# Kernel tuning notes

Hardware: AMD Instinct MI355X
Metric: run time of the kernel (lower is better)

## Reference

```python
import jax, jax.numpy as jnp
import numpy as np

B, R, T, D = 16, 1024, 512, 1024
H = 1024  # hidden_dim

def setup_inputs() -> dict:
    key = jax.random.key(0)
    ks = jax.random.split(key, 8)
    s_in = 1.0 / np.sqrt(D)
    s_comb = 1.0 / np.sqrt(3 * D)
    return {
        "region_feats": jax.random.normal(ks[0], (B, R, D), jnp.float32),
        "query_embs": jax.random.normal(ks[1], (B, T, D), jnp.float32),
        "Wr": jax.random.normal(ks[2], (D, H), jnp.float32) * s_in,
        "br": jnp.zeros((H,), jnp.float32),
        "Wq": jax.random.normal(ks[3], (D, H), jnp.float32) * s_in,
        "bq": jnp.zeros((H,), jnp.float32),
        "Ws": jax.random.normal(ks[4], (3 * D, 1), jnp.float32) * s_comb,
        "bs": jnp.zeros((1,), jnp.float32),
    }

def reference(region_feats, query_embs, Wr, br, Wq, bq, Ws, bs):
    # Dense projections
    R_proj = region_feats @ Wr + br            # [B,R,H]
    Q_proj = query_embs @ Wq + bq              # [B,T,H]
    # Unscaled cross-attention scores
    scores = jnp.einsum('brd,btd->brt', R_proj, Q_proj)  # [B,R,T]
    attn = jax.nn.softmax(scores, axis=-1)
    # Attend over RAW query embeddings (as in source)
    attended = jnp.einsum('brt,btd->brd', attn, query_embs)  # [B,R,D]
    combined = jnp.concatenate(
        [region_feats, attended, region_feats * attended], axis=-1)  # [B,R,3D]
    out = combined @ Ws + bs                    # [B,R,1]
    return jnp.squeeze(out, axis=-1)            # [B,R]
```

## Files before the change

### kernel.cpp

```cpp
#include <hip/hip_runtime.h>


#define BD 16
#define RD 1024
#define TD 512
#define DD 1024
#define BR (BD * RD)

typedef _Float16 half8 __attribute__((ext_vector_type(8)));
typedef _Float16 half4 __attribute__((ext_vector_type(4)));
typedef float floatx4 __attribute__((ext_vector_type(4)));

__device__ __forceinline__ float wave_sum(float v) {
#pragma unroll
  for (int off = 32; off > 0; off >>= 1) v += __shfl_down(v, off);
  return v;
}

__device__ __forceinline__ half8 cvt8(float4 a, float4 b) {
  half8 h = {(_Float16)a.x, (_Float16)a.y, (_Float16)a.z, (_Float16)a.w,
             (_Float16)b.x, (_Float16)b.y, (_Float16)b.z, (_Float16)b.w};
  return h;
}

__device__ __forceinline__ void gl16(const _Float16* g, _Float16* l) {
  __builtin_amdgcn_global_load_lds(
      (const __attribute__((address_space(1))) void*)g,
      (__attribute__((address_space(3))) void*)l, 16, 0, 0);
}

__global__ __launch_bounds__(256) void prep_all(
    const float* __restrict__ Wr, const float* __restrict__ Wq,
    const float* __restrict__ Ws, const float* __restrict__ br,
    const float* __restrict__ region, const float* __restrict__ query,
    _Float16* __restrict__ M2, _Float16* __restrict__ Ws16,
    float* __restrict__ wqbr, _Float16* __restrict__ wqbr16,
    _Float16* __restrict__ r16, float* __restrict__ rdvec,
    _Float16* __restrict__ q16, float* __restrict__ h1) {
  __shared__ __align__(16) _Float16 lds[2 * 2 * 2048];
  __shared__ float sm[4];
  const int blk = blockIdx.x, tid = threadIdx.x;

  if (blk < 256) {
    const int m0 = (blk >> 4) * 64, n0 = (blk & 15) * 64;
    const int lane = tid & 63, w = tid >> 6;
    const int wr = w >> 1, wc = w & 1;
    const int srow = tid >> 2, slot = tid & 3;
    const int scol = (slot ^ ((srow >> 1) & 3)) * 8;
    const long offA = (long)(m0 + srow) * DD + scol;
    const long offB = (long)(n0 + srow) * DD + scol;
    const int wofs = srow * 32 + slot * 8;
    const int NK = DD / 32;
    float4 a0, a1, b0, b1;
    a0 = *(const float4*)(Wr + offA); a1 = *(const float4*)(Wr + offA + 4);
    b0 = *(const float4*)(Wq + offB); b1 = *(const float4*)(Wq + offB + 4);
    *(int4*)&lds[wofs] = *(int4*)&(const half8&)cvt8(a0, a1);
    {
      half8 hb = cvt8(b0, b1);
      *(half8*)&lds[2048 + wofs] = hb;
    }
    a0 = *(const float4*)(Wr + offA + 32); a1 = *(const float4*)(Wr + offA + 36);
    b0 = *(const float4*)(Wq + offB + 32); b1 = *(const float4*)(Wq + offB + 36);
    __syncthreads();
    floatx4 acc[2][2] = {};
    const int fr = lane & 15, g = lane >> 4;
    const int fs = (g ^ ((fr >> 1) & 3)) * 8;
    for (int kt = 0; kt < NK; ++kt) {
      const int cur = (kt & 1) * 4096, nxt = ((kt + 1) & 1) * 4096;
      if (kt + 1 < NK) {
        half8 ha = cvt8(a0, a1), hb = cvt8(b0, b1);
        *(half8*)&lds[nxt + wofs] = ha;
        *(half8*)&lds[nxt + 2048 + wofs] = hb;
      }
      if (kt + 2 < NK) {
        const long go = (long)(kt + 2) * 32;
        a0 = *(const float4*)(Wr + offA + go); a1 = *(const float4*)(Wr + offA + go + 4);
        b0 = *(const float4*)(Wq + offB + go); b1 = *(const float4*)(Wq + offB + go + 4);
      }
      half8 af[2], bf[2];
#pragma unroll
      for (int i = 0; i < 2; ++i)
        af[i] = *(const half8*)&lds[cur + (32 * wr + 16 * i + fr) * 32 + fs];
#pragma unroll
      for (int j = 0; j < 2; ++j)
        bf[j] = *(const half8*)&lds[cur + 2048 + (32 * wc + 16 * j + fr) * 32 + fs];
#pragma unroll
      for (int i = 0; i < 2; ++i)
#pragma unroll
        for (int j = 0; j < 2; ++j)
          acc[i][j] = __builtin_amdgcn_mfma_f32_16x16x32_f16(af[i], bf[j], acc[i][j], 0, 0, 0);
      __syncthreads();
    }
    const int cr = g * 4, cc = fr;
#pragma unroll
    for (int i = 0; i < 2; ++i)
#pragma unroll
      for (int r = 0; r < 4; ++r)
#pragma unroll
        for (int j = 0; j < 2; ++j)
          M2[(long)(m0 + 32 * wr + 16 * i + cr + r) * DD + n0 + 32 * wc + 16 * j + cc] =
              (_Float16)acc[i][j][r];
  } else if (blk < 258) {
    const long i = (long)(blk - 256) * 1024 + tid * 4;
    const float4 v = *(const float4*)&Ws[DD + i];
    half4 h = {(_Float16)v.x, (_Float16)v.y, (_Float16)v.z, (_Float16)v.w};
    *(half4*)&Ws16[i] = h;
  } else if (blk < 514) {
    const int row = (blk - 258) * 4 + (tid >> 6);
    const int lane = tid & 63;
    const float* x = Wq + (long)row * DD;
    float s = 0.f;
    for (int k = lane; k < DD; k += 64) s += x[k] * br[k];
    s = wave_sum(s);
    if (lane == 0) {
      wqbr[row] = s;
      wqbr16[row] = (_Float16)s;
    }
  } else if (blk < 514 + BR) {
    const long row = blk - 514;
    const int lane = tid & 63, wid = tid >> 6;
    const long i = row * DD + tid * 4;
    const float4 v = *(const float4*)&region[i];
    half4 h = {(_Float16)v.x, (_Float16)v.y, (_Float16)v.z, (_Float16)v.w};
    *(half4*)&r16[i] = h;
    const float4 w0 = *(const float4*)&Ws[tid * 4];
    float rd = v.x * w0.x + v.y * w0.y + v.z * w0.z + v.w * w0.w;
    rd = wave_sum(rd);
    if (lane == 0) sm[wid] = rd;
    __syncthreads();
    if (tid == 0) rdvec[row] = sm[0] + sm[1] + sm[2] + sm[3];
  } else {
    const long row = blk - (514 + BR);
    const int lane = tid & 63, wid = tid >> 6;
    const long i = row * DD + tid * 4;
    const float4 v = *(const float4*)&query[i];
    half4 h = {(_Float16)v.x, (_Float16)v.y, (_Float16)v.z, (_Float16)v.w};
    *(half4*)&q16[i] = h;
    const float4 w1 = *(const float4*)&Ws[DD + tid * 4];
    float hq = v.x * w1.x + v.y * w1.y + v.z * w1.z + v.w * w1.w;
    hq = wave_sum(hq);
    if (lane == 0) sm[wid] = hq;
    __syncthreads();
    if (tid == 0) h1[row] = sm[0] + sm[1] + sm[2] + sm[3];
  }
}

__global__ __launch_bounds__(512, 4) void qp_gemm(
    const _Float16* __restrict__ A, const _Float16* __restrict__ B,
    _Float16* __restrict__ C, const _Float16* __restrict__ wq16,
    float* __restrict__ cvec) {
  __shared__ __align__(16) _Float16 lds[2 * 2 * 4096];
  const int lin = blockIdx.x;
  const int s = lin & 7, u = lin >> 3;
  const int mt = s * 8 + (u >> 3), nt = u & 7;
  const int m0 = mt * 128, n0 = nt * 128;
  const int tid = threadIdx.x, lane = tid & 63, w = tid >> 6;
  const int wr = w >> 1, wc = w & 1;

  const int lrow = lane >> 2, slot = lane & 3;
  const int scol = (slot ^ ((lrow >> 1) & 3)) * 8;
  const int srow = 16 * w + lrow;
  const _Float16* gA = A + (long)(m0 + srow) * DD + scol;
  const _Float16* gB = B + (long)(n0 + srow) * DD + scol;
  const int wbase = 512 * w;

  gl16(gA, &lds[wbase]);
  gl16(gB, &lds[4096 + wbase]);
  __syncthreads();

  floatx4 acc[2][4] = {};
  float cvp[2] = {0.f, 0.f};
  const int fr = lane & 15, g = lane >> 4;
  const int fs = (g ^ ((fr >> 1) & 3)) * 8;
  const int NK = DD / 32;

  for (int kt = 0; kt < NK; ++kt) {
    const int cur = (kt & 1) * 8192, nxt = cur ^ 8192;
    if (kt + 1 < NK) {
      const long go = (long)(kt + 1) * 32;
      gl16(gA + go, &lds[nxt + wbase]);
      gl16(gB + go, &lds[nxt + 4096 + wbase]);
    }
    half8 af[2], bf[4];
#pragma unroll
    for (int i = 0; i < 2; ++i)
      af[i] = *(const half8*)&lds[cur + (32 * wr + 16 * i + fr) * 32 + fs];
#pragma unroll
    for (int j = 0; j < 4; ++j)
      bf[j] = *(const half8*)&lds[cur + 4096 + (64 * wc + 16 * j + fr) * 32 + fs];
    if (wc == 0) {
      const half8 wb = *(const half8*)&wq16[kt * 32 + g * 8];
#pragma unroll
      for (int i = 0; i < 2; ++i)
#pragma unroll
        for (int e = 0; e < 8; ++e)
          cvp[i] += (float)af[i][e] * (float)wb[e];
    }
#pragma unroll
    for (int i = 0; i < 2; ++i)
#pragma unroll
      for (int j = 0; j < 4; ++j)
        acc[i][j] = __builtin_amdgcn_mfma_f32_16x16x32_f16(af[i], bf[j], acc[i][j], 0, 0, 0);
    __syncthreads();
  }

  if (wc == 0 && nt == 0) {
#pragma unroll
    for (int i = 0; i < 2; ++i) {
      float c = cvp[i];
      c += __shfl_xor(c, 16);
      c += __shfl_xor(c, 32);
      if (lane < 16) cvec[m0 + 32 * wr + 16 * i + lane] = c;
    }
  }

  const int cr = g * 4, cc = fr;
#pragma unroll
  for (int i = 0; i < 2; ++i)
#pragma unroll
    for (int r = 0; r < 4; ++r)
#pragma unroll
      for (int j = 0; j < 4; ++j)
        C[(long)(m0 + 32 * wr + 16 * i + cr + r) * DD + n0 + 64 * wc + 16 * j + cc] =
            (_Float16)acc[i][j][r];
}

__global__ __launch_bounds__(512, 4) void gemm_fused(
    const _Float16* __restrict__ A, const _Float16* __restrict__ B0,
    const _Float16* __restrict__ B1,
    float* __restrict__ Ms, float* __restrict__ Ls, float* __restrict__ Hs,
    const float* __restrict__ cvec, const float* __restrict__ h1,
    const _Float16* __restrict__ wsh, long sA, long sB) {
  __shared__ __align__(16) _Float16 lds[2 * 3 * 4096];
  __shared__ __align__(16) _Float16 wlds[1024];

  const int lin = blockIdx.x;
  const int s = lin & 7, u = lin >> 3;
  const int b = 2 * s + (u >> 5);
  const int t = u & 31;
  const int mt = t >> 2, nt = t & 3;
  const int m0 = mt * 128, n0 = nt * 128;
  A += (long)b * sA;
  B0 += (long)b * sB;
  B1 += (long)b * sB;

  const int tid = threadIdx.x, lane = tid & 63, w = tid >> 6;
  const int wr = w >> 2, wc = w & 3;

  const int lrow = lane >> 2, slot = lane & 3;
  const int scol = (slot ^ ((lrow >> 1) & 3)) * 8;
  const int srow = 16 * w + lrow;
  const _Float16* gA = A + (long)(m0 + srow) * DD + scol;
  const _Float16* gP = B0 + (long)(n0 + srow) * DD + scol;
  const _Float16* gQ = B1 + (long)(n0 + srow) * DD + scol;
  const int wbase = 512 * w;

  if (tid < 128) *(int4*)&wlds[tid * 8] = *(const int4*)&wsh[1024 + tid * 8];

  gl16(gA, &lds[wbase]);
  gl16(gP, &lds[4096 + wbase]);
  gl16(gQ, &lds[8192 + wbase]);
  __syncthreads();

  floatx4 accS[4][2] = {};
  floatx4 accH[4][2] = {};
  const int fr = lane & 15, g = lane >> 4;
  const int fs = (g ^ ((fr >> 1) & 3)) * 8;
  const int NK = DD / 32;

  for (int kt = 0; kt < NK; ++kt) {
    const int cur = (kt & 1) * 12288;
    const int nxt = cur ^ 12288;
    if (kt + 1 < NK) {
      const long go = (long)(kt + 1) * 32;
      gl16(gA + go, &lds[nxt + wbase]);
      gl16(gP + go, &lds[nxt + 4096 + wbase]);
      gl16(gQ + go, &lds[nxt + 8192 + wbase]);
    }
    half8 af[4], bp[2], bq[2];
#pragma unroll
    for (int i = 0; i < 4; ++i)
      af[i] = *(const half8*)&lds[cur + (64 * wr + 16 * i + fr) * 32 + fs];
#pragma unroll
    for (int j = 0; j < 2; ++j)
      bp[j] = *(const half8*)&lds[cur + 4096 + (32 * wc + 16 * j + fr) * 32 + fs];
#pragma unroll
    for (int j = 0; j < 2; ++j)
      bq[j] = *(const half8*)&lds[cur + 8192 + (32 * wc + 16 * j + fr) * 32 + fs];
    const half8 w2f = *(const half8*)&wlds[kt * 32 + g * 8];
#pragma unroll
    for (int j = 0; j < 2; ++j) bq[j] *= w2f;
#pragma unroll
    for (int i = 0; i < 4; ++i)
#pragma unroll
      for (int j = 0; j < 2; ++j)
        accS[i][j] = __builtin_amdgcn_mfma_f32_16x16x32_f16(af[i], bp[j], accS[i][j], 0, 0, 0);
#pragma unroll
    for (int i = 0; i < 4; ++i)
#pragma unroll
      for (int j = 0; j < 2; ++j)
        accH[i][j] = __builtin_amdgcn_mfma_f32_16x16x32_f16(af[i], bq[j], accH[i][j], 0, 0, 0);
    __syncthreads();
  }

  const int cr = g * 4, cc = fr;
  float cv[2], hv[2];
#pragma unroll
  for (int j = 0; j < 2; ++j) {
    const long col = (long)b * TD + n0 + 32 * wc + 16 * j + cc;
    cv[j] = cvec[col];
    hv[j] = h1[col];
  }
  const int chunk = nt * 4 + wc;
  const long rowBase = (long)b * RD + m0 + 64 * wr + cr;
#pragma unroll
  for (int i = 0; i < 4; ++i) {
#pragma unroll
    for (int r = 0; r < 4; ++r) {
      float mx = fmaxf(accS[i][0][r] + cv[0], accS[i][1][r] + cv[1]);
      mx = fmaxf(mx, __shfl_xor(mx, 1));
      mx = fmaxf(mx, __shfl_xor(mx, 2));
      mx = fmaxf(mx, __shfl_xor(mx, 4));
      mx = fmaxf(mx, __shfl_xor(mx, 8));
      float l = 0.f, hs = 0.f;
#pragma unroll
      for (int j = 0; j < 2; ++j) {
        const float e = __expf(accS[i][j][r] + cv[j] - mx);
        l += e;
        hs += e * (accH[i][j][r] + hv[j]);
      }
      l += __shfl_xor(l, 1); hs += __shfl_xor(hs, 1);
      l += __shfl_xor(l, 2); hs += __shfl_xor(hs, 2);
      l += __shfl_xor(l, 4); hs += __shfl_xor(hs, 4);
      l += __shfl_xor(l, 8); hs += __shfl_xor(hs, 8);
      if (cc == 0) {
        const long idx = (long)chunk * BR + rowBase + 16 * i + r;
        Ms[idx] = mx;
        Ls[idx] = l;
        Hs[idx] = hs;
      }
    }
  }
}

__global__ __launch_bounds__(256) void combine(
    const float* __restrict__ Ms, const float* __restrict__ Ls,
    const float* __restrict__ Hs, const float* __restrict__ rdvec,
    const float* __restrict__ bs, float* __restrict__ out) {
  const int row = blockIdx.x * 256 + threadIdx.x;
  float mv[16];
  float gm = -1e30f;
#pragma unroll
  for (int c = 0; c < 16; ++c) {
    mv[c] = Ms[(long)c * BR + row];
    gm = fmaxf(gm, mv[c]);
  }
  float L = 0.f, HS = 0.f;
#pragma unroll
  for (int c = 0; c < 16; ++c) {
    const float sc = __expf(mv[c] - gm);
    L += Ls[(long)c * BR + row] * sc;
    HS += Hs[(long)c * BR + row] * sc;
  }
  out[row] = HS / L + rdvec[row] + bs[0];
}

extern "C" void kernel_launch(void* const* d_in, const int* in_sizes, int n_in,
                              void* d_out, int out_size, void* d_ws, size_t ws_size,
                              hipStream_t stream) {
  const float* region = (const float*)d_in[0];
  const float* query  = (const float*)d_in[1];
  const float* Wr     = (const float*)d_in[2];
  const float* br     = (const float*)d_in[3];
  const float* Wq     = (const float*)d_in[4];
  const float* Ws     = (const float*)d_in[6];
  const float* bs     = (const float*)d_in[7];
  float* out = (float*)d_out;

  char* p = (char*)d_ws;
  _Float16* region16 = (_Float16*)p;
  _Float16* query16  = (_Float16*)(p + (32u << 20));
  _Float16* Qp       = (_Float16*)(p + (48u << 20));
  _Float16* M2       = (_Float16*)(p + (64u << 20));
  _Float16* Ws16     = (_Float16*)(p + (66u << 20));
  float*    wqbr     = (float*)(p + (66u << 20) + 8192);
  _Float16* wqbr16   = (_Float16*)(p + (66u << 20) + 12288);
  float*    cvec     = (float*)(p + (66u << 20) + 16384);
  float*    rdvec    = (float*)(p + (66u << 20) + 65536);
  float*    h1       = (float*)(p + (66u << 20) + 131072);
  float*    Ms       = (float*)(p + (67u << 20));
  float*    Ls       = Ms + 16 * BR;
  float*    Hs       = Ls + 16 * BR;

  prep_all<<<dim3(514 + BR + BD * TD), 256, 0, stream>>>(
      Wr, Wq, Ws, br, region, query, M2, Ws16, wqbr, wqbr16,
      region16, rdvec, query16, h1);
  qp_gemm<<<dim3(512), 512, 0, stream>>>(query16, M2, Qp, wqbr16, cvec);
  gemm_fused<<<dim3(512), 512, 0, stream>>>(
      region16, Qp, query16, Ms, Ls, Hs, cvec, h1, Ws16,
      (long)RD * DD, (long)TD * DD);
  combine<<<dim3(BR / 256), 256, 0, stream>>>(Ms, Ls, Hs, rdvec, bs, out);
}
```

Before: 218.0 us.

## Deepen fused GEMM pipeline to four LDS stages and batch prep rows per wave

The fused score/attention GEMM moves from a double-buffered LDS loop to a four-stage ring. It uses explicit vmcnt waits, raw barriers and MFMA priority bumps so global-to-LDS loads run three k-steps ahead. LDS use grows to about 96KB per block and occupancy hint drops to 2 blocks per CU. Separately, the fp16 conversion and dot-product prep now handles one row per wave instead of one per block, which cuts block count and removes shared-memory reductions and block syncs.

Result: slower. 227.3 us (+4.3%).

```diff
diff --git a/kernel.cpp b/kernel.cpp
--- a/kernel.cpp
+++ b/kernel.cpp
@@ -38,7 +38,6 @@
     _Float16* __restrict__ r16, float* __restrict__ rdvec,
     _Float16* __restrict__ q16, float* __restrict__ h1) {
   __shared__ __align__(16) _Float16 lds[2 * 2 * 2048];
-  __shared__ float sm[4];
   const int blk = blockIdx.x, tid = threadIdx.x;
 
   if (blk < 256) {
@@ -116,32 +115,40 @@
       wqbr[row] = s;
       wqbr16[row] = (_Float16)s;
     }
-  } else if (blk < 514 + BR) {
-    const long row = blk - 514;
-    const int lane = tid & 63, wid = tid >> 6;
-    const long i = row * DD + tid * 4;
-    const float4 v = *(const float4*)&region[i];
-    half4 h = {(_Float16)v.x, (_Float16)v.y, (_Float16)v.z, (_Float16)v.w};
-    *(half4*)&r16[i] = h;
-    const float4 w0 = *(const float4*)&Ws[tid * 4];
-    float rd = v.x * w0.x + v.y * w0.y + v.z * w0.z + v.w * w0.w;
+  } else if (blk < 514 + BR / 4) {
+    const int wid = tid >> 6, lane = tid & 63;
+    const long row = (long)(blk - 514) * 4 + wid;
+    const float* src = region + row * DD;
+    _Float16* dst = r16 + row * DD;
+    float rd = 0.f;
+#pragma unroll
+    for (int it = 0; it < 4; ++it) {
+      const int c = it * 256 + lane * 4;
+      const float4 v = *(const float4*)&src[c];
+      const float4 w0 = *(const float4*)&Ws[c];
+      half4 h = {(_Float16)v.x, (_Float16)v.y, (_Float16)v.z, (_Float16)v.w};
+      *(half4*)&dst[c] = h;
+      rd += v.x * w0.x + v.y * w0.y + v.z * w0.z + v.w * w0.w;
+    }
     rd = wave_sum(rd);
-    if (lane == 0) sm[wid] = rd;
-    __syncthreads();
-    if (tid == 0) rdvec[row] = sm[0] + sm[1] + sm[2] + sm[3];
+    if (lane == 0) rdvec[row] = rd;
   } else {
-    const long row = blk - (514 + BR);
-    const int lane = tid & 63, wid = tid >> 6;
-    const long i = row * DD + tid * 4;
-    const float4 v = *(const float4*)&query[i];
-    half4 h = {(_Float16)v.x, (_Float16)v.y, (_Float16)v.z, (_Float16)v.w};
-    *(half4*)&q16[i] = h;
-    const float4 w1 = *(const float4*)&Ws[DD + tid * 4];
-    float hq = v.x * w1.x + v.y * w1.y + v.z * w1.z + v.w * w1.w;
+    const int wid = tid >> 6, lane = tid & 63;
+    const long row = (long)(blk - (514 + BR / 4)) * 4 + wid;
+    const float* src = query + row * DD;
+    _Float16* dst = q16 + row * DD;
+    float hq = 0.f;
+#pragma unroll
+    for (int it = 0; it < 4; ++it) {
+      const int c = it * 256 + lane * 4;
+      const float4 v = *(const float4*)&src[c];
+      const float4 w1 = *(const float4*)&Ws[DD + c];
+      half4 h = {(_Float16)v.x, (_Float16)v.y, (_Float16)v.z, (_Float16)v.w};
+      *(half4*)&dst[c] = h;
+      hq += v.x * w1.x + v.y * w1.y + v.z * w1.z + v.w * w1.w;
+    }
     hq = wave_sum(hq);
-    if (lane == 0) sm[wid] = hq;
-    __syncthreads();
-    if (tid == 0) h1[row] = sm[0] + sm[1] + sm[2] + sm[3];
+    if (lane == 0) h1[row] = hq;
   }
 }
 
@@ -225,13 +232,48 @@
             (_Float16)acc[i][j][r];
 }
 
-__global__ __launch_bounds__(512, 4) void gemm_fused(
+#define STAGE3(hh, sl)                                    \
+  {                                                       \
+    const long go_ = (long)(hh) * 32;                     \
+    gl16(gA + go_, &lds[(sl) * 12288 + wbase]);           \
+    gl16(gP + go_, &lds[(sl) * 12288 + 4096 + wbase]);    \
+    gl16(gQ + go_, &lds[(sl) * 12288 + 8192 + wbase]);    \
+  }
+
+#define HALFSTEP(h, sl, VM)                                                    \
+  {                                                                            \
+    asm volatile("s_waitcnt vmcnt(" #VM ")" ::: "memory");                     \
+    __builtin_amdgcn_s_barrier();                                              \
+    asm volatile("" ::: "memory");                                             \
+    half8 af[4], bp[2], bq[2];                                                 \
+    _Pragma("unroll") for (int i = 0; i < 4; ++i)                              \
+      af[i] = *(const half8*)&lds[(sl) * 12288 + (64 * wr + 16 * i + fr) * 32 + fs]; \
+    _Pragma("unroll") for (int j = 0; j < 2; ++j)                              \
+      bp[j] = *(const half8*)&lds[(sl) * 12288 + 4096 + (32 * wc + 16 * j + fr) * 32 + fs]; \
+    _Pragma("unroll") for (int j = 0; j < 2; ++j)                              \
+      bq[j] = *(const half8*)&lds[(sl) * 12288 + 8192 + (32 * wc + 16 * j + fr) * 32 + fs]; \
+    const half8 w2f = *(const half8*)&wlds[(h) * 32 + g * 8];                  \
+    bq[0] *= w2f;                                                              \
+    bq[1] *= w2f;                                                              \
+    __builtin_amdgcn_s_setprio(1);                                             \
+    _Pragma("unroll") for (int i = 0; i < 4; ++i)                              \
+      _Pragma("unroll") for (int j = 0; j < 2; ++j)                            \
+        accS[i][j] = __builtin_amdgcn_mfma_f32_16x16x32_f16(af[i], bp[j], accS[i][j], 0, 0, 0); \
+    _Pragma("unroll") for (int i = 0; i < 4; ++i)                              \
+      _Pragma("unroll") for (int j = 0; j < 2; ++j)                            \
+        accH[i][j] = __builtin_amdgcn_mfma_f32_16x16x32_f16(af[i], bq[j], accH[i][j], 0, 0, 0); \
+    __builtin_amdgcn_s_setprio(0);                                             \
+    __builtin_amdgcn_s_barrier();                                              \
+    asm volatile("" ::: "memory");                                             \
+  }
+
+__global__ __launch_bounds__(512, 2) void gemm_fused(
     const _Float16* __restrict__ A, const _Float16* __restrict__ B0,
     const _Float16* __restrict__ B1,
     float* __restrict__ Ms, float* __restrict__ Ls, float* __restrict__ Hs,
     const float* __restrict__ cvec, const float* __restrict__ h1,
     const _Float16* __restrict__ wsh, long sA, long sB) {
-  __shared__ __align__(16) _Float16 lds[2 * 3 * 4096];
+  __shared__ __align__(16) _Float16 lds[4 * 12288];
   __shared__ __align__(16) _Float16 wlds[1024];
 
   const int lin = blockIdx.x;
@@ -256,52 +298,27 @@
   const int wbase = 512 * w;
 
   if (tid < 128) *(int4*)&wlds[tid * 8] = *(const int4*)&wsh[1024 + tid * 8];
-
-  gl16(gA, &lds[wbase]);
-  gl16(gP, &lds[4096 + wbase]);
-  gl16(gQ, &lds[8192 + wbase]);
   __syncthreads();
 
   floatx4 accS[4][2] = {};
   floatx4 accH[4][2] = {};
   const int fr = lane & 15, g = lane >> 4;
   const int fs = (g ^ ((fr >> 1) & 3)) * 8;
-  const int NK = DD / 32;
-
-  for (int kt = 0; kt < NK; ++kt) {
-    const int cur = (kt & 1) * 12288;
-    const int nxt = cur ^ 12288;
-    if (kt + 1 < NK) {
-      const long go = (long)(kt + 1) * 32;
-      gl16(gA + go, &lds[nxt + wbase]);
-      gl16(gP + go, &lds[nxt + 4096 + wbase]);
-      gl16(gQ + go, &lds[nxt + 8192 + wbase]);
-    }
-    half8 af[4], bp[2], bq[2];
-#pragma unroll
-    for (int i = 0; i < 4; ++i)
-      af[i] = *(const half8*)&lds[cur + (64 * wr + 16 * i + fr) * 32 + fs];
-#pragma unroll
-    for (int j = 0; j < 2; ++j)
-      bp[j] = *(const half8*)&lds[cur + 4096 + (32 * wc + 16 * j + fr) * 32 + fs];
-#pragma unroll
-    for (int j = 0; j < 2; ++j)
-      bq[j] = *(const half8*)&lds[cur + 8192 + (32 * wc + 16 * j + fr) * 32 + fs];
-    const half8 w2f = *(const half8*)&wlds[kt * 32 + g * 8];
-#pragma unroll
-    for (int j = 0; j < 2; ++j) bq[j] *= w2f;
-#pragma unroll
-    for (int i = 0; i < 4; ++i)
-#pragma unroll
-      for (int j = 0; j < 2; ++j)
-        accS[i][j] = __builtin_amdgcn_mfma_f32_16x16x32_f16(af[i], bp[j], accS[i][j], 0, 0, 0);
-#pragma unroll
-    for (int i = 0; i < 4; ++i)
-#pragma unroll
-      for (int j = 0; j < 2; ++j)
-        accH[i][j] = __builtin_amdgcn_mfma_f32_16x16x32_f16(af[i], bq[j], accH[i][j], 0, 0, 0);
-    __syncthreads();
-  }
+
+  STAGE3(0, 0);
+  STAGE3(1, 1);
+  STAGE3(2, 2);
+
+  for (int hb = 0; hb < 28; hb += 4) {
+    STAGE3(hb + 3, 3); HALFSTEP(hb + 0, 0, 9);
+    STAGE3(hb + 4, 0); HALFSTEP(hb + 1, 1, 9);
+    STAGE3(hb + 5, 1); HALFSTEP(hb + 2, 2, 9);
+    STAGE3(hb + 6, 2); HALFSTEP(hb + 3, 3, 9);
+  }
+  STAGE3(31, 3); HALFSTEP(28, 0, 9);
+  HALFSTEP(29, 1, 6);
+  HALFSTEP(30, 2, 3);
+  HALFSTEP(31, 3, 0);
 
   const int cr = g * 4, cc = fr;
   float cv[2], hv[2];
@@ -392,7 +409,7 @@
   float*    Ls       = Ms + 16 * BR;
   float*    Hs       = Ls + 16 * BR;
 
-  prep_all<<<dim3(514 + BR + BD * TD), 256, 0, stream>>>(
+  prep_all<<<dim3(514 + BR / 4 + BD * TD / 4), 256, 0, stream>>>(
       Wr, Wq, Ws, br, region, query, M2, Ws16, wqbr, wqbr16,
       region16, rdvec, query16, h1);
   qp_gemm<<<dim3(512), 512, 0, stream>>>(query16, M2, Qp, wqbr16, cvec);
```
